# Performance work log

Hardware: AMD Instinct MI355X
Metric: run time of the kernel (lower is better)

Reference implementation:

```python
import jax, jax.numpy as jnp
import numpy as np
import math

D_MODEL = 768
NUM_HEADS = 12
HEAD_SIZE = D_MODEL // NUM_HEADS
BATCH = 4
SEQ = 2048


def setup_inputs() -> dict:
    key = jax.random.key(0)
    ks = jax.random.split(key, 11)
    s = 1.0 / math.sqrt(D_MODEL)
    inp = {
        "queries": jax.random.normal(ks[0], (BATCH, SEQ, D_MODEL), jnp.float32),
        "keys": jax.random.normal(ks[1], (BATCH, SEQ, D_MODEL), jnp.float32),
        "values": jax.random.normal(ks[2], (BATCH, SEQ, D_MODEL), jnp.float32),
        # nn.Linear weights are (out_features, in_features); y = x @ W.T + b
        "W_Q": jax.random.uniform(ks[3], (D_MODEL, D_MODEL), jnp.float32, -s, s),
        "b_Q": jax.random.uniform(ks[4], (D_MODEL,), jnp.float32, -s, s),
        "W_K": jax.random.uniform(ks[5], (D_MODEL, D_MODEL), jnp.float32, -s, s),
        "b_K": jax.random.uniform(ks[6], (D_MODEL,), jnp.float32, -s, s),
        "W_V": jax.random.uniform(ks[7], (D_MODEL, D_MODEL), jnp.float32, -s, s),
        "b_V": jax.random.uniform(ks[8], (D_MODEL,), jnp.float32, -s, s),
        "W_O": jax.random.uniform(ks[9], (D_MODEL, D_MODEL), jnp.float32, -s, s),
        "b_O": jax.random.uniform(ks[10], (D_MODEL,), jnp.float32, -s, s),
    }
    return inp


def _split_heads(x):
    # [B, S, H*d] -> [B, H, S, d]
    B, S, _ = x.shape
    return x.reshape(B, S, NUM_HEADS, HEAD_SIZE).transpose(0, 2, 1, 3)


def _merge_heads(x):
    # [B, H, S, d] -> [B, S, H*d]
    B, H, S, d = x.shape
    return x.transpose(0, 2, 1, 3).reshape(B, S, H * d)


def reference(queries, keys, values, W_Q, b_Q, W_K, b_K, W_V, b_V, W_O, b_O):
    Q = _split_heads(queries @ W_Q.T + b_Q)  # [B,H,S,d]
    K = _split_heads(keys @ W_K.T + b_K)
    V = _split_heads(values @ W_V.T + b_V)

    scale = 1.0 / math.sqrt(HEAD_SIZE)
    scores = jnp.einsum("bhqd,bhkd->bhqk", Q, K) * scale  # [B,H,S,S]
    causal = jnp.tril(jnp.ones((SEQ, SEQ), dtype=bool))  # [S,S]
    scores = jnp.where(causal, scores, -jnp.inf)
    attn = jax.nn.softmax(scores, axis=-1)  # causal weights, zeros above diag
    attended = jnp.einsum("bhqk,bhkd->bhqd", attn, V)
    context = _merge_heads(attended)  # [B,S,D]
    outputs = context @ W_O.T + b_O
    return outputs
```

## Files before the change

kernel.cpp:

```cpp
#include <hip/hip_runtime.h>
#include <hip/hip_bf16.h>

#define DM 768
#define NH 12
#define HD 64
#define B_ 4
#define S_ 2048
#define MT (B_*S_)

typedef unsigned short u16;
typedef __attribute__((ext_vector_type(8))) short bf16x8;
typedef __attribute__((ext_vector_type(4))) float f32x4;
typedef __attribute__((ext_vector_type(4))) short s16x4;
typedef __attribute__((ext_vector_type(4))) unsigned u32x4;

__device__ __forceinline__ u16 f2bf(float f) {
    union { float f; unsigned u; } x; x.f = f;
    unsigned r = x.u + 0x7fffu + ((x.u >> 16) & 1u);
    return (u16)(r >> 16);
}

__device__ __forceinline__ unsigned pk2(float a, float b) {
    union { __hip_bfloat162 h; unsigned u; } cv;
    cv.h = __float22bfloat162_rn(float2{a, b});
    return cv.u;
}

__device__ __forceinline__ void swap32(unsigned& a, unsigned& b) {
    asm volatile("v_permlane32_swap_b32 %0, %1" : "+v"(a), "+v"(b));
}
__device__ __forceinline__ void swap16(unsigned& a, unsigned& b) {
    asm volatile("v_permlane16_swap_b32 %0, %1" : "+v"(a), "+v"(b));
}

#define GLD_LDS(gp, lp) \
    __builtin_amdgcn_global_load_lds( \
        (const __attribute__((address_space(1))) void*)(gp), \
        (__attribute__((address_space(3))) void*)(lp), 16, 0, 0)

__global__ void cvt3_kernel(const float* __restrict__ s0, const float* __restrict__ s1,
                            const float* __restrict__ s2,
                            u16* __restrict__ d0, u16* __restrict__ d1, u16* __restrict__ d2,
                            int blocksPer) {
    int sel = blockIdx.x / blocksPer;
    int rel = blockIdx.x % blocksPer;
    const float* s = (sel == 0) ? s0 : (sel == 1) ? s1 : s2;
    u16* d = (sel == 0) ? d0 : (sel == 1) ? d1 : d2;
    int i = (rel * 256 + threadIdx.x) * 4;
    float4 v = *(const float4*)(s + i);
    s16x4 o;
    o.x = (short)f2bf(v.x); o.y = (short)f2bf(v.y);
    o.z = (short)f2bf(v.z); o.w = (short)f2bf(v.w);
    *(s16x4*)(d + i) = o;
}

__global__ void cvt4_kernel(const float* __restrict__ s0, const float* __restrict__ s1,
                            const float* __restrict__ s2, const float* __restrict__ s3,
                            u16* __restrict__ d0, u16* __restrict__ d1,
                            u16* __restrict__ d2, u16* __restrict__ d3,
                            int blocksPer) {
    int sel = blockIdx.x / blocksPer;
    int rel = blockIdx.x % blocksPer;
    const float* s = (sel == 0) ? s0 : (sel == 1) ? s1 : (sel == 2) ? s2 : s3;
    u16* d = (sel == 0) ? d0 : (sel == 1) ? d1 : (sel == 2) ? d2 : d3;
    int i = (rel * 256 + threadIdx.x) * 4;
    float4 v = *(const float4*)(s + i);
    s16x4 o;
    o.x = (short)f2bf(v.x); o.y = (short)f2bf(v.y);
    o.z = (short)f2bf(v.z); o.w = (short)f2bf(v.w);
    *(s16x4*)(d + i) = o;
}

__device__ __forceinline__ void gemm_core_128(
    const u16* __restrict__ A, const u16* __restrict__ B,
    int m0, int n0, u16* As, u16* Bs, f32x4 acc[4][4])
{
    const int tid = threadIdx.x;
    const int lane = tid & 63;
    const int lr = lane & 15, quad = lane >> 4;
    const int wave = tid >> 6;
    const int wm = (wave & 1) * 64, wn = (wave >> 1) * 64;

    for (int ks = 0; ks < 24; ++ks) {
        #pragma unroll
        for (int r = 0; r < 2; ++r) {
            int idx = r * 256 + tid;
            int row = idx >> 2, col = (idx & 3) * 8;
            GLD_LDS(A + (size_t)(m0 + row) * DM + ks * 32 + col, As + idx * 8);
            GLD_LDS(B + (size_t)(n0 + row) * DM + ks * 32 + col, Bs + idx * 8);
        }
        __syncthreads();
        bf16x8 a[4], b[4];
        #pragma unroll
        for (int i = 0; i < 4; ++i) a[i] = *(const bf16x8*)(As + (wm + i * 16 + lr) * 32 + quad * 8);
        #pragma unroll
        for (int j = 0; j < 4; ++j) b[j] = *(const bf16x8*)(Bs + (wn + j * 16 + lr) * 32 + quad * 8);
        #pragma unroll
        for (int i = 0; i < 4; ++i)
            #pragma unroll
            for (int j = 0; j < 4; ++j)
                acc[i][j] = __builtin_amdgcn_mfma_f32_16x16x32_bf16(a[i], b[j], acc[i][j], 0, 0, 0);
        __syncthreads();
    }
}

__global__ __launch_bounds__(256) void qkv_gemm(
    const u16* __restrict__ Xq, const u16* __restrict__ Xk, const u16* __restrict__ Xv,
    const u16* __restrict__ Wq, const u16* __restrict__ Wk, const u16* __restrict__ Wv,
    const float* __restrict__ bQ, const float* __restrict__ bK, const float* __restrict__ bV,
    u16* __restrict__ Qo, u16* __restrict__ Ko, u16* __restrict__ VTo)
{
    __shared__ __align__(16) u16 As[128 * 32];
    __shared__ __align__(16) u16 Bs[128 * 32];

    const int mat = blockIdx.x / 384;
    const int t   = blockIdx.x % 384;
    const int mt  = t / 6, nt = t % 6;
    const u16* X = (mat == 0) ? Xq : (mat == 1 ? Xk : Xv);
    const u16* W = (mat == 0) ? Wq : (mat == 1 ? Wk : Wv);
    const float* bias = (mat == 0) ? bQ : (mat == 1 ? bK : bV);

    const int lane = threadIdx.x & 63;
    const int lr = lane & 15, quad = lane >> 4;
    const int wave = threadIdx.x >> 6;
    const int m0 = mt * 128 + (wave & 1) * 64;
    const int n0 = nt * 128 + (wave >> 1) * 64;

    f32x4 acc[4][4] = {};
    gemm_core_128(X, W, mt * 128, nt * 128, As, Bs, acc);

    const int bb = m0 / S_, s0 = m0 % S_, h = n0 / HD;
    if (mat < 2) {
        u16* O = (mat == 0) ? Qo : Ko;
        const float qs = (mat == 0) ? 0.18033688011112042f : 1.0f;
        #pragma unroll
        for (int jj = 0; jj < 4; ++jj) {
            float bv = bias[n0 + jj * 16 + lr];
            #pragma unroll
            for (int i = 0; i < 4; ++i)
                #pragma unroll
                for (int r = 0; r < 4; ++r) {
                    int s = s0 + i * 16 + quad * 4 + r;
                    O[((size_t)(bb * NH + h) * S_ + s) * HD + jj * 16 + lr] = f2bf((acc[i][jj][r] + bv) * qs);
                }
        }
    } else {
        #pragma unroll
        for (int jj = 0; jj < 4; ++jj) {
            float bv = bias[n0 + jj * 16 + lr];
            #pragma unroll
            for (int i = 0; i < 4; ++i) {
                int s = s0 + i * 16 + quad * 4;
                s16x4 o;
                o.x = (short)f2bf(acc[i][jj][0] + bv);
                o.y = (short)f2bf(acc[i][jj][1] + bv);
                o.z = (short)f2bf(acc[i][jj][2] + bv);
                o.w = (short)f2bf(acc[i][jj][3] + bv);
                *(s16x4*)(VTo + ((size_t)(bb * NH + h) * HD + jj * 16 + lr) * S_ + s) = o;
            }
        }
    }
}

__global__ __launch_bounds__(256, 3) void attn_kernel(
    const u16* __restrict__ Q, const u16* __restrict__ K,
    const u16* __restrict__ VT, u16* __restrict__ CTX)
{
    const int tid = threadIdx.x;
    const int wave = tid >> 6;
    const int lane = tid & 63;
    const int lr = lane & 15, quad = lane >> 4;
    const int xcd = blockIdx.x & 7;
    const int idx = blockIdx.x >> 3;
    const int bh  = xcd * 6 + (idx % 6);
    const int qw  = 63 - (idx / 6);
    const int q0  = qw * 32;
    const u16* Qb = Q  + (size_t)bh * S_ * HD;
    const u16* Kb = K  + (size_t)bh * S_ * HD;
    const u16* Vb = VT + (size_t)bh * HD * S_;

    __shared__ __align__(16) float smem[2 * 64 * 44];

    bf16x8 aq[2][2];
    #pragma unroll
    for (int mi = 0; mi < 2; ++mi)
        #pragma unroll
        for (int kk = 0; kk < 2; ++kk)
            aq[mi][kk] = *(const bf16x8*)(Qb + (size_t)(q0 + mi * 16 + lr) * HD + kk * 32 + quad * 8);

    f32x4 o[2][4] = {};
    f32x4 lacc[2] = {};
    bf16x8 ones;
    #pragma unroll
    for (int j = 0; j < 8; ++j) ones[j] = (short)0x3F80;

    const int ktmax = (q0 + 31) >> 6;

    for (int kt = wave; kt <= ktmax; kt += 4) {
        const int k0 = kt << 6;

        bf16x8 bk[4][2];
        #pragma unroll
        for (int nt = 0; nt < 4; ++nt)
            #pragma unroll
            for (int kk = 0; kk < 2; ++kk)
                bk[nt][kk] = *(const bf16x8*)(Kb + (size_t)(k0 + nt * 16 + lr) * HD + kk * 32 + quad * 8);

        f32x4 sT[2][4];
        #pragma unroll
        for (int mi = 0; mi < 2; ++mi)
            #pragma unroll
            for (int t = 0; t < 4; ++t) {
                f32x4 z = {0.f, 0.f, 0.f, 0.f};
                z = __builtin_amdgcn_mfma_f32_16x16x32_bf16(bk[t][0], aq[mi][0], z, 0, 0, 0);
                z = __builtin_amdgcn_mfma_f32_16x16x32_bf16(bk[t][1], aq[mi][1], z, 0, 0, 0);
                sT[mi][t] = z;
            }

        if (kt == ktmax) {
            #pragma unroll
            for (int mi = 0; mi < 2; ++mi) {
                int qrow = q0 + mi * 16 + lr;
                #pragma unroll
                for (int t = 0; t < 4; ++t)
                    #pragma unroll
                    for (int r = 0; r < 4; ++r) {
                        int key = k0 + t * 16 + quad * 4 + r;
                        if (key > qrow) sT[mi][t][r] = -INFINITY;
                    }
            }
        }

        bf16x8 bv[4][2];
        #pragma unroll
        for (int nv = 0; nv < 4; ++nv)
            #pragma unroll
            for (int c = 0; c < 2; ++c)
                bv[nv][c] = *(const bf16x8*)(Vb + (size_t)(nv * 16 + lr) * S_ + k0 + c * 32 + quad * 8);

        bf16x8 pa[2][2];
        #pragma unroll
        for (int mi = 0; mi < 2; ++mi) {
            #pragma unroll
            for (int t = 0; t < 4; ++t)
                #pragma unroll
                for (int r = 0; r < 4; ++r)
                    sT[mi][t][r] = exp2f(sT[mi][t][r]);

            #pragma unroll
            for (int c = 0; c < 2; ++c) {
                unsigned u00 = pk2(sT[mi][2 * c + 0][0], sT[mi][2 * c + 0][1]);
                unsigned u01 = pk2(sT[mi][2 * c + 0][2], sT[mi][2 * c + 0][3]);
                unsigned u10 = pk2(sT[mi][2 * c + 1][0], sT[mi][2 * c + 1][1]);
                unsigned u11 = pk2(sT[mi][2 * c + 1][2], sT[mi][2 * c + 1][3]);
                swap32(u00, u10); swap16(u00, u10);
                swap32(u01, u11); swap16(u01, u11);
                u32x4 P = {u00, u01, u10, u11};
                pa[mi][c] = __builtin_bit_cast(bf16x8, P);
            }
        }

        #pragma unroll
        for (int mi = 0; mi < 2; ++mi) {
            lacc[mi] = __builtin_amdgcn_mfma_f32_16x16x32_bf16(pa[mi][0], ones, lacc[mi], 0, 0, 0);
            lacc[mi] = __builtin_amdgcn_mfma_f32_16x16x32_bf16(pa[mi][1], ones, lacc[mi], 0, 0, 0);
            #pragma unroll
            for (int nv = 0; nv < 4; ++nv) {
                o[mi][nv] = __builtin_amdgcn_mfma_f32_16x16x32_bf16(pa[mi][0], bv[nv][0], o[mi][nv], 0, 0, 0);
                o[mi][nv] = __builtin_amdgcn_mfma_f32_16x16x32_bf16(pa[mi][1], bv[nv][1], o[mi][nv], 0, 0, 0);
            }
        }
    }

    __syncthreads();
    float* red = smem;
    if (wave >= 2) {
        float* rp = red + (wave - 2) * (64 * 44) + lane * 44;
        #pragma unroll
        for (int mi = 0; mi < 2; ++mi) {
            #pragma unroll
            for (int nv = 0; nv < 4; ++nv)
                *(f32x4*)(rp + (mi * 4 + nv) * 4) = o[mi][nv];
            *(f32x4*)(rp + 32 + mi * 4) = lacc[mi];
        }
    }
    __syncthreads();
    if (wave < 2) {
        const float* rp = red + wave * (64 * 44) + lane * 44;
        #pragma unroll
        for (int mi = 0; mi < 2; ++mi) {
            #pragma unroll
            for (int nv = 0; nv < 4; ++nv)
                o[mi][nv] += *(const f32x4*)(rp + (mi * 4 + nv) * 4);
            lacc[mi] += *(const f32x4*)(rp + 32 + mi * 4);
        }
    }
    __syncthreads();
    if (wave == 1) {
        float* rp = red + lane * 44;
        #pragma unroll
        for (int mi = 0; mi < 2; ++mi) {
            #pragma unroll
            for (int nv = 0; nv < 4; ++nv)
                *(f32x4*)(rp + (mi * 4 + nv) * 4) = o[mi][nv];
            *(f32x4*)(rp + 32 + mi * 4) = lacc[mi];
        }
    }
    __syncthreads();
    if (wave == 0) {
        const float* rp = red + lane * 44;
        #pragma unroll
        for (int mi = 0; mi < 2; ++mi) {
            #pragma unroll
            for (int nv = 0; nv < 4; ++nv)
                o[mi][nv] += *(const f32x4*)(rp + (mi * 4 + nv) * 4);
            lacc[mi] += *(const f32x4*)(rp + 32 + mi * 4);
        }
        const int bb = bh / NH, h = bh % NH;
        #pragma unroll
        for (int mi = 0; mi < 2; ++mi) {
            f32x4 inv;
            #pragma unroll
            for (int r = 0; r < 4; ++r) inv[r] = 1.0f / lacc[mi][r];
            #pragma unroll
            for (int nv = 0; nv < 4; ++nv)
                #pragma unroll
                for (int r = 0; r < 4; ++r)
                    CTX[(size_t)(bb * S_ + q0 + mi * 16 + quad * 4 + r) * DM + h * HD + nv * 16 + lr]
                        = f2bf(o[mi][nv][r] * inv[r]);
        }
    }
}

__global__ __launch_bounds__(256) void o_gemm(
    const u16* __restrict__ X, const u16* __restrict__ W,
    const float* __restrict__ bias, float* __restrict__ Out)
{
    __shared__ __align__(16) u16 As[128 * 32];
    __shared__ __align__(16) u16 Bs[128 * 32];

    const int mt = blockIdx.x / 6, nt = blockIdx.x % 6;
    const int lane = threadIdx.x & 63;
    const int lr = lane & 15, quad = lane >> 4;
    const int wave = threadIdx.x >> 6;
    const int m0 = mt * 128 + (wave & 1) * 64;
    const int n0 = nt * 128 + (wave >> 1) * 64;

    f32x4 acc[4][4] = {};
    gemm_core_128(X, W, mt * 128, nt * 128, As, Bs, acc);

    #pragma unroll
    for (int jj = 0; jj < 4; ++jj) {
        float bv = bias[n0 + jj * 16 + lr];
        #pragma unroll
        for (int i = 0; i < 4; ++i)
            #pragma unroll
            for (int r = 0; r < 4; ++r)
                Out[(size_t)(m0 + i * 16 + quad * 4 + r) * DM + n0 + jj * 16 + lr] = acc[i][jj][r] + bv;
    }
}

extern "C" void kernel_launch(void* const* d_in, const int* in_sizes, int n_in,
                              void* d_out, int out_size, void* d_ws, size_t ws_size,
                              hipStream_t stream) {
    const float* q  = (const float*)d_in[0];
    const float* k  = (const float*)d_in[1];
    const float* v  = (const float*)d_in[2];
    const float* WQ = (const float*)d_in[3];
    const float* bQ = (const float*)d_in[4];
    const float* WK = (const float*)d_in[5];
    const float* bK = (const float*)d_in[6];
    const float* WV = (const float*)d_in[7];
    const float* bV = (const float*)d_in[8];
    const float* WO = (const float*)d_in[9];
    const float* bO = (const float*)d_in[10];

    char* ws = (char*)d_ws;
    const size_t SZ_X = (size_t)MT * DM * 2;
    const size_t SZ_W = (size_t)DM * DM * 2;
    u16* Xq = (u16*)(ws);
    u16* Xk = (u16*)(ws + SZ_X);
    u16* Xv = (u16*)(ws + 2 * SZ_X);
    u16* Wq = (u16*)(ws + 3 * SZ_X);
    u16* Wk = (u16*)(ws + 3 * SZ_X + SZ_W);
    u16* Wv = (u16*)(ws + 3 * SZ_X + 2 * SZ_W);
    u16* Wo = (u16*)(ws + 3 * SZ_X + 3 * SZ_W);
    u16* Qh  = (u16*)(ws + 3 * SZ_X + 4 * SZ_W);
    u16* Kh  = (u16*)(ws + 4 * SZ_X + 4 * SZ_W);
    u16* VTh = (u16*)(ws + 5 * SZ_X + 4 * SZ_W);
    u16* CTX = Xq;

    const int nX = MT * DM;
    const int nW = DM * DM;
    cvt3_kernel<<<3 * (nX / 1024), 256, 0, stream>>>(q, k, v, Xq, Xk, Xv, nX / 1024);
    cvt4_kernel<<<4 * (nW / 1024), 256, 0, stream>>>(WQ, WK, WV, WO, Wq, Wk, Wv, Wo, nW / 1024);

    qkv_gemm<<<1152, 256, 0, stream>>>(Xq, Xk, Xv, Wq, Wk, Wv, bQ, bK, bV, Qh, Kh, VTh);
    attn_kernel<<<3072, 256, 0, stream>>>(Qh, Kh, VTh, CTX);
    o_gemm<<<384, 256, 0, stream>>>(CTX, Wo, bO, (float*)d_out);
}
```

Baseline: 316.2 us.

## Share double-buffered K/V tiles in LDS across waves owning separate query rows

The attention kernel is restructured so each block covers 128 query rows, with each wave owning 32 rows. Previously each wave took a different key tile for the same 32 queries and the partial results were reduced through shared memory. Now all waves in a block iterate over the same key tiles, which are staged into XOR-swizzled LDS buffers with direct global-to-LDS loads and double buffering. This cuts redundant global K/V reads and removes the cross-wave reduction. In exchange the grid shrinks to a quarter, each iteration adds a block-wide barrier, and under the causal mask waves with earlier query rows sit idle on the final tiles.

```diff
diff --git a/kernel.cpp b/kernel.cpp
--- a/kernel.cpp
+++ b/kernel.cpp
@@ -170,23 +170,27 @@
     const int wave = tid >> 6;
     const int lane = tid & 63;
     const int lr = lane & 15, quad = lane >> 4;
+
     const int xcd = blockIdx.x & 7;
-    const int idx = blockIdx.x >> 3;
-    const int bh  = xcd * 6 + (idx % 6);
-    const int qw  = 63 - (idx / 6);
-    const int q0  = qw * 32;
+    const int i2  = blockIdx.x >> 3;
+    const int bh  = xcd * 6 + (i2 % 6);
+    const int qc  = 15 - (i2 / 6);
+    const int Q0  = qc * 128;
+    const int q0w = Q0 + wave * 32;
+
     const u16* Qb = Q  + (size_t)bh * S_ * HD;
     const u16* Kb = K  + (size_t)bh * S_ * HD;
     const u16* Vb = VT + (size_t)bh * HD * S_;
 
-    __shared__ __align__(16) float smem[2 * 64 * 44];
+    __shared__ __align__(16) u16 kbuf[2][64 * 64];
+    __shared__ __align__(16) u16 vbuf[2][64 * 64];
 
     bf16x8 aq[2][2];
     #pragma unroll
     for (int mi = 0; mi < 2; ++mi)
         #pragma unroll
         for (int kk = 0; kk < 2; ++kk)
-            aq[mi][kk] = *(const bf16x8*)(Qb + (size_t)(q0 + mi * 16 + lr) * HD + kk * 32 + quad * 8);
+            aq[mi][kk] = *(const bf16x8*)(Qb + (size_t)(q0w + mi * 16 + lr) * HD + kk * 32 + quad * 8);
 
     f32x4 o[2][4] = {};
     f32x4 lacc[2] = {};
@@ -194,141 +198,125 @@
     #pragma unroll
     for (int j = 0; j < 8; ++j) ones[j] = (short)0x3F80;
 
-    const int ktmax = (q0 + 31) >> 6;
-
-    for (int kt = wave; kt <= ktmax; kt += 4) {
-        const int k0 = kt << 6;
-
-        bf16x8 bk[4][2];
-        #pragma unroll
-        for (int nt = 0; nt < 4; ++nt)
-            #pragma unroll
-            for (int kk = 0; kk < 2; ++kk)
-                bk[nt][kk] = *(const bf16x8*)(Kb + (size_t)(k0 + nt * 16 + lr) * HD + kk * 32 + quad * 8);
-
-        f32x4 sT[2][4];
-        #pragma unroll
-        for (int mi = 0; mi < 2; ++mi)
-            #pragma unroll
-            for (int t = 0; t < 4; ++t) {
-                f32x4 z = {0.f, 0.f, 0.f, 0.f};
-                z = __builtin_amdgcn_mfma_f32_16x16x32_bf16(bk[t][0], aq[mi][0], z, 0, 0, 0);
-                z = __builtin_amdgcn_mfma_f32_16x16x32_bf16(bk[t][1], aq[mi][1], z, 0, 0, 0);
-                sT[mi][t] = z;
+    const int KT  = 2 * qc + 1;
+    const int ktw = (q0w + 31) >> 6;
+
+#define STAGE_KV(b, kk0) do {                                                   \
+        _Pragma("unroll")                                                       \
+        for (int j = 0; j < 2; ++j) {                                           \
+            int ch  = ((j * 4 + wave) << 6) + lane;                             \
+            int row = ch >> 3;                                                  \
+            int cl  = (ch & 7) ^ (row & 7);                                     \
+            GLD_LDS(Kb + (size_t)((kk0) + row) * HD + cl * 8, &kbuf[b][ch * 8]);\
+            GLD_LDS(Vb + (size_t)row * S_ + (kk0) + cl * 8, &vbuf[b][ch * 8]);  \
+        }                                                                       \
+    } while (0)
+
+    STAGE_KV(0, 0);
+    __syncthreads();
+
+    for (int kt = 0; kt <= KT; ++kt) {
+        const int cur = kt & 1;
+        if (kt < KT) STAGE_KV(cur ^ 1, (kt + 1) << 6);
+
+        if (kt <= ktw) {
+            const int k0 = kt << 6;
+
+            bf16x8 bk[4][2];
+            #pragma unroll
+            for (int t = 0; t < 4; ++t)
+                #pragma unroll
+                for (int kk = 0; kk < 2; ++kk) {
+                    int row = t * 16 + lr;
+                    int cp  = (kk * 4 + quad) ^ (row & 7);
+                    bk[t][kk] = *(const bf16x8*)(&kbuf[cur][row * 64 + cp * 8]);
+                }
+
+            f32x4 sT[2][4];
+            #pragma unroll
+            for (int mi = 0; mi < 2; ++mi)
+                #pragma unroll
+                for (int t = 0; t < 4; ++t) {
+                    f32x4 z = {0.f, 0.f, 0.f, 0.f};
+                    z = __builtin_amdgcn_mfma_f32_16x16x32_bf16(bk[t][0], aq[mi][0], z, 0, 0, 0);
+                    z = __builtin_amdgcn_mfma_f32_16x16x32_bf16(bk[t][1], aq[mi][1], z, 0, 0, 0);
+                    sT[mi][t] = z;
+                }
+
+            if (kt == ktw) {
+                #pragma unroll
+                for (int mi = 0; mi < 2; ++mi) {
+                    int qrow = q0w + mi * 16 + lr;
+                    #pragma unroll
+                    for (int t = 0; t < 4; ++t)
+                        #pragma unroll
+                        for (int r = 0; r < 4; ++r) {
+                            int key = k0 + t * 16 + quad * 4 + r;
+                            if (key > qrow) sT[mi][t][r] = -INFINITY;
+                        }
+                }
             }
 
-        if (kt == ktmax) {
+            bf16x8 bv[4][2];
+            #pragma unroll
+            for (int nv = 0; nv < 4; ++nv)
+                #pragma unroll
+                for (int c2 = 0; c2 < 2; ++c2) {
+                    int row = nv * 16 + lr;
+                    int cp  = (c2 * 4 + quad) ^ (row & 7);
+                    bv[nv][c2] = *(const bf16x8*)(&vbuf[cur][row * 64 + cp * 8]);
+                }
+
+            bf16x8 pa[2][2];
             #pragma unroll
             for (int mi = 0; mi < 2; ++mi) {
-                int qrow = q0 + mi * 16 + lr;
                 #pragma unroll
                 for (int t = 0; t < 4; ++t)
                     #pragma unroll
-                    for (int r = 0; r < 4; ++r) {
-                        int key = k0 + t * 16 + quad * 4 + r;
-                        if (key > qrow) sT[mi][t][r] = -INFINITY;
-                    }
+                    for (int r = 0; r < 4; ++r)
+                        sT[mi][t][r] = exp2f(sT[mi][t][r]);
+
+                #pragma unroll
+                for (int c = 0; c < 2; ++c) {
+                    unsigned u00 = pk2(sT[mi][2 * c + 0][0], sT[mi][2 * c + 0][1]);
+                    unsigned u01 = pk2(sT[mi][2 * c + 0][2], sT[mi][2 * c + 0][3]);
+                    unsigned u10 = pk2(sT[mi][2 * c + 1][0], sT[mi][2 * c + 1][1]);
+                    unsigned u11 = pk2(sT[mi][2 * c + 1][2], sT[mi][2 * c + 1][3]);
+                    swap32(u00, u10); swap16(u00, u10);
+                    swap32(u01, u11); swap16(u01, u11);
+                    u32x4 P = {u00, u01, u10, u11};
+                    pa[mi][c] = __builtin_bit_cast(bf16x8, P);
+                }
+            }
+
+            #pragma unroll
+            for (int mi = 0; mi < 2; ++mi) {
+                lacc[mi] = __builtin_amdgcn_mfma_f32_16x16x32_bf16(pa[mi][0], ones, lacc[mi], 0, 0, 0);
+                lacc[mi] = __builtin_amdgcn_mfma_f32_16x16x32_bf16(pa[mi][1], ones, lacc[mi], 0, 0, 0);
+                #pragma unroll
+                for (int nv = 0; nv < 4; ++nv) {
+                    o[mi][nv] = __builtin_amdgcn_mfma_f32_16x16x32_bf16(pa[mi][0], bv[nv][0], o[mi][nv], 0, 0, 0);
+                    o[mi][nv] = __builtin_amdgcn_mfma_f32_16x16x32_bf16(pa[mi][1], bv[nv][1], o[mi][nv], 0, 0, 0);
+                }
             }
         }
 
-        bf16x8 bv[4][2];
+        __syncthreads();
+    }
+#undef STAGE_KV
+
+    const int bb = bh / NH, h = bh % NH;
+    #pragma unroll
+    for (int mi = 0; mi < 2; ++mi) {
+        f32x4 inv;
+        #pragma unroll
+        for (int r = 0; r < 4; ++r) inv[r] = 1.0f / lacc[mi][r];
         #pragma unroll
         for (int nv = 0; nv < 4; ++nv)
             #pragma unroll
-            for (int c = 0; c < 2; ++c)
-                bv[nv][c] = *(const bf16x8*)(Vb + (size_t)(nv * 16 + lr) * S_ + k0 + c * 32 + quad * 8);
-
-        bf16x8 pa[2][2];
-        #pragma unroll
-        for (int mi = 0; mi < 2; ++mi) {
-            #pragma unroll
-            for (int t = 0; t < 4; ++t)
-                #pragma unroll
-                for (int r = 0; r < 4; ++r)
-                    sT[mi][t][r] = exp2f(sT[mi][t][r]);
-
-            #pragma unroll
-            for (int c = 0; c < 2; ++c) {
-                unsigned u00 = pk2(sT[mi][2 * c + 0][0], sT[mi][2 * c + 0][1]);
-                unsigned u01 = pk2(sT[mi][2 * c + 0][2], sT[mi][2 * c + 0][3]);
-                unsigned u10 = pk2(sT[mi][2 * c + 1][0], sT[mi][2 * c + 1][1]);
-                unsigned u11 = pk2(sT[mi][2 * c + 1][2], sT[mi][2 * c + 1][3]);
-                swap32(u00, u10); swap16(u00, u10);
-                swap32(u01, u11); swap16(u01, u11);
-                u32x4 P = {u00, u01, u10, u11};
-                pa[mi][c] = __builtin_bit_cast(bf16x8, P);
-            }
-        }
-
-        #pragma unroll
-        for (int mi = 0; mi < 2; ++mi) {
-            lacc[mi] = __builtin_amdgcn_mfma_f32_16x16x32_bf16(pa[mi][0], ones, lacc[mi], 0, 0, 0);
-            lacc[mi] = __builtin_amdgcn_mfma_f32_16x16x32_bf16(pa[mi][1], ones, lacc[mi], 0, 0, 0);
-            #pragma unroll
-            for (int nv = 0; nv < 4; ++nv) {
-                o[mi][nv] = __builtin_amdgcn_mfma_f32_16x16x32_bf16(pa[mi][0], bv[nv][0], o[mi][nv], 0, 0, 0);
-                o[mi][nv] = __builtin_amdgcn_mfma_f32_16x16x32_bf16(pa[mi][1], bv[nv][1], o[mi][nv], 0, 0, 0);
-            }
-        }
-    }
-
-    __syncthreads();
-    float* red = smem;
-    if (wave >= 2) {
-        float* rp = red + (wave - 2) * (64 * 44) + lane * 44;
-        #pragma unroll
-        for (int mi = 0; mi < 2; ++mi) {
-            #pragma unroll
-            for (int nv = 0; nv < 4; ++nv)
-                *(f32x4*)(rp + (mi * 4 + nv) * 4) = o[mi][nv];
-            *(f32x4*)(rp + 32 + mi * 4) = lacc[mi];
-        }
-    }
-    __syncthreads();
-    if (wave < 2) {
-        const float* rp = red + wave * (64 * 44) + lane * 44;
-        #pragma unroll
-        for (int mi = 0; mi < 2; ++mi) {
-            #pragma unroll
-            for (int nv = 0; nv < 4; ++nv)
-                o[mi][nv] += *(const f32x4*)(rp + (mi * 4 + nv) * 4);
-            lacc[mi] += *(const f32x4*)(rp + 32 + mi * 4);
-        }
-    }
-    __syncthreads();
-    if (wave == 1) {
-        float* rp = red + lane * 44;
-        #pragma unroll
-        for (int mi = 0; mi < 2; ++mi) {
-            #pragma unroll
-            for (int nv = 0; nv < 4; ++nv)
-                *(f32x4*)(rp + (mi * 4 + nv) * 4) = o[mi][nv];
-            *(f32x4*)(rp + 32 + mi * 4) = lacc[mi];
-        }
-    }
-    __syncthreads();
-    if (wave == 0) {
-        const float* rp = red + lane * 44;
-        #pragma unroll
-        for (int mi = 0; mi < 2; ++mi) {
-            #pragma unroll
-            for (int nv = 0; nv < 4; ++nv)
-                o[mi][nv] += *(const f32x4*)(rp + (mi * 4 + nv) * 4);
-            lacc[mi] += *(const f32x4*)(rp + 32 + mi * 4);
-        }
-        const int bb = bh / NH, h = bh % NH;
-        #pragma unroll
-        for (int mi = 0; mi < 2; ++mi) {
-            f32x4 inv;
-            #pragma unroll
-            for (int r = 0; r < 4; ++r) inv[r] = 1.0f / lacc[mi][r];
-            #pragma unroll
-            for (int nv = 0; nv < 4; ++nv)
-                #pragma unroll
-                for (int r = 0; r < 4; ++r)
-                    CTX[(size_t)(bb * S_ + q0 + mi * 16 + quad * 4 + r) * DM + h * HD + nv * 16 + lr]
-                        = f2bf(o[mi][nv][r] * inv[r]);
-        }
+            for (int r = 0; r < 4; ++r)
+                CTX[(size_t)(bb * S_ + q0w + mi * 16 + quad * 4 + r) * DM + h * HD + nv * 16 + lr]
+                    = f2bf(o[mi][nv][r] * inv[r]);
     }
 }
 
@@ -396,6 +384,6 @@
     cvt4_kernel<<<4 * (nW / 1024), 256, 0, stream>>>(WQ, WK, WV, WO, Wq, Wk, Wv, Wo, nW / 1024);
 
     qkv_gemm<<<1152, 256, 0, stream>>>(Xq, Xk, Xv, Wq, Wk, Wv, bQ, bK, bV, Qh, Kh, VTh);
-    attn_kernel<<<3072, 256, 0, stream>>>(Qh, Kh, VTh, CTX);
+    attn_kernel<<<768, 256, 0, stream>>>(Qh, Kh, VTh, CTX);
     o_gemm<<<384, 256, 0, stream>>>(CTX, Wo, bO, (float*)d_out);
 }
```

Measured after the change: 274.9 us. 1.15x faster.
